# Kernel tuning notes

Hardware: AMD Instinct MI355X
Metric: run time of the kernel (lower is better)

The kernel has to match this reference:

```python
import jax, jax.numpy as jnp
import numpy as np

H, W = 512, 512          # resized_image_size
HEAT_R = 40              # heatmap_radius
OFF_R = 40               # offsetmap_radius
N_PTS = 19               # num landmarks (channels // 3)
B = 4


def _general_maps():
    # heatmap: binary disk of radius HEAT_R centered at (H, W) on a (2H, 2W) grid
    yg = jnp.arange(2 * H)[:, None]
    xg = jnp.arange(2 * W)[None, :]
    dist2 = ((yg - H) ** 2 + (xg - W) ** 2).astype(jnp.float32)
    heat = (jnp.sqrt(dist2) <= HEAT_R).astype(jnp.float32)
    # offsetmap_x: (H - row_index) / OFF_R, broadcast along columns
    off_x = jnp.broadcast_to(
        (H - jnp.arange(2 * H, dtype=jnp.float32))[:, None] / OFF_R, (2 * H, 2 * W))
    # offsetmap_y: (W - col_index) / OFF_R, broadcast along rows
    off_y = jnp.broadcast_to(
        (W - jnp.arange(2 * W, dtype=jnp.float32))[None, :] / OFF_R, (2 * H, 2 * W))
    return heat, off_x, off_y


def _crop(source, x, y):
    # rect[b, n, i, j] = source[H - y[b,n] + i, W - x[b,n] + j]
    row = (H - y)[:, :, :] if False else (H - y)[:, :, None] + jnp.arange(H)  # [B, N, H]
    col = (W - x)[:, :, None] + jnp.arange(W)                                # [B, N, W]
    return source[row[:, :, :, None], col[:, :, None, :]]                    # [B, N, H, W]


def setup_inputs() -> dict:
    key = jax.random.key(0)
    k1, k2 = jax.random.split(key)
    feature_maps = jax.random.normal(k1, (B, 3 * N_PTS, H, W), dtype=jnp.float32)
    landmarks = jax.random.randint(k2, (B, N_PTS, 2), 0, 512, dtype=jnp.int32)
    return {"feature_maps": feature_maps, "landmarks": landmarks}


def reference(feature_maps, landmarks):
    heat_map, off_x_map, off_y_map = _general_maps()
    lm = landmarks.astype(jnp.int32)
    x = jnp.clip(lm[..., 0], 1, W - 1)   # clamp_landmarks
    y = jnp.clip(lm[..., 1], 1, H - 1)

    heatmaps = _crop(heat_map, x, y)     # [B, N, H, W]
    offmap_x = _crop(off_x_map, x, y)
    offmap_y = _crop(off_y_map, x, y)

    # mask = (clamped landmarks > 0).prod(-1); always 1 after clamp but kept faithful
    mask = ((x > 0) & (y > 0)).astype(jnp.float32)[:, :, None, None]

    n = N_PTS
    ph, th = feature_maps[:, :n] * mask, heatmaps * mask
    px, tx = feature_maps[:, n:2 * n] * mask, offmap_x * mask
    py, ty = feature_maps[:, 2 * n:] * mask, offmap_y * mask

    # BCE with logits, mean reduction (numerically stable form)
    bce = jnp.mean(jnp.maximum(ph, 0.0) - ph * th + jnp.log1p(jnp.exp(-jnp.abs(ph))))

    # L1 over elements where target heatmap > 0 (masked-mean form, jit-safe)
    ind = (th > 0).astype(jnp.float32)
    cnt = jnp.sum(ind)
    lx = jnp.sum(jnp.abs(px - tx) * ind) / cnt
    ly = jnp.sum(jnp.abs(py - ty) * ind) / cnt

    return 2.0 * bce + lx + ly
```

## Files before the change

kernel.cpp:

```cpp
#include <hip/hip_runtime.h>
#include <math.h>

static constexpr int H = 512, W = 512, NPTS = 19, BATCH = 4;
static constexpr int HW = H * W;
static constexpr int NPLANES = BATCH * NPTS;
static constexpr long long TOTAL = (long long)NPLANES * HW;
static constexpr float INV_OFF = 1.0f / 40.0f;

static constexpr int BX_BULK = 16;
static constexpr int BX_DISK = 8;
static constexpr int BX      = BX_BULK + BX_DISK;
static constexpr int SITER   = (HW / 4) / (BX_BULK * 256);
static constexpr int NBULK   = BX_BULK * NPLANES;
static constexpr int NDISK   = BX_DISK * NPLANES;

__global__ __launch_bounds__(256) void homl_main(
    const float* __restrict__ fm, const int* __restrict__ lm,
    double* __restrict__ ws_)
{
    const int bn = blockIdx.y;
    const int b  = bn / NPTS;
    const int n  = bn % NPTS;

    int x = lm[bn * 2 + 0];
    int y = lm[bn * 2 + 1];
    x = min(max(x, 1), W - 1);
    y = min(max(y, 1), H - 1);

    __shared__ float redf[4][4];
    const int wave = threadIdx.x >> 6;
    const int lane = threadIdx.x & 63;

    if (blockIdx.x < BX_BULK) {
        const float* ph_base = fm + ((size_t)b * 3 * NPTS + n) * HW;
        const int v0 = blockIdx.x * (SITER * 256) + threadIdx.x;

        float bce = 0.0f;
        float4 buf[4];
        #pragma unroll
        for (int s0 = 0; s0 < 3; ++s0)
            buf[s0] = *reinterpret_cast<const float4*>(ph_base + (v0 + s0 * 256) * 4);

        #pragma unroll
        for (int s = 0; s < SITER; ++s) {
            if (s + 3 < SITER)
                buf[(s + 3) & 3] = *reinterpret_cast<const float4*>(
                    ph_base + (v0 + (s + 3) * 256) * 4);

            const int p   = (v0 + s * 256) * 4;
            const int i   = p >> 9;
            const int j   = p & (W - 1);
            const int dy  = i - y;
            const int dy2 = dy * dy;

            const float pha[4] = {buf[s & 3].x, buf[s & 3].y, buf[s & 3].z, buf[s & 3].w};
            #pragma unroll
            for (int k = 0; k < 4; ++k) {
                const int dx = j + k - x;
                const int d2 = dy2 + dx * dx;
                const float ph = pha[k];
                const float a  = fabsf(ph);
                const float sp = 0.69314718056f *
                                 log2f(1.0f + exp2f(-1.44269504089f * a));
                bce += fmaxf(ph, 0.0f) + sp;
                bce -= (d2 <= 1600) ? ph : 0.0f;
            }
        }

        #pragma unroll
        for (int off = 32; off > 0; off >>= 1) bce += __shfl_down(bce, off);
        if (lane == 0) redf[0][wave] = bce;
        __syncthreads();
        if (threadIdx.x == 0) {
            double db = 0.0;
            #pragma unroll
            for (int wv = 0; wv < 4; ++wv) db += (double)redf[0][wv];
            ws_[bn * BX_BULK + blockIdx.x] = db;
        }
    } else {
        const int dblk = blockIdx.x - BX_BULK;
        const float* px_base = fm + ((size_t)b * 3 * NPTS + NPTS + n) * HW;
        const float* py_base = fm + ((size_t)b * 3 * NPTS + 2 * NPTS + n) * HW;

        const int rbeg = dblk * 11;
        const int rcnt = min(11, 81 - rbeg);

        float lxs = 0.0f, lys = 0.0f, cntf = 0.0f;
        for (int idx = threadIdx.x; idx < rcnt * 81; idx += 256) {
            const int rr = idx / 81;
            const int cc = idx - rr * 81;
            const int dy = rbeg + rr - 40;
            const int dx = cc - 40;
            const int r  = y + dy;
            const int c  = x + dx;
            if (r >= 0 && r < H && c >= 0 && c < W && dy * dy + dx * dx <= 1600) {
                const float tx = (float)(-dy) * INV_OFF;
                const float ty = (float)(-dx) * INV_OFF;
                const size_t off = (size_t)r * W + c;
                lxs  += fabsf(px_base[off] - tx);
                lys  += fabsf(py_base[off] - ty);
                cntf += 1.0f;
            }
        }

        #pragma unroll
        for (int off = 32; off > 0; off >>= 1) {
            lxs  += __shfl_down(lxs, off);
            lys  += __shfl_down(lys, off);
            cntf += __shfl_down(cntf, off);
        }
        if (lane == 0) { redf[1][wave] = lxs; redf[2][wave] = lys; redf[3][wave] = cntf; }
        __syncthreads();
        if (threadIdx.x == 0) {
            double dxs = 0.0, dys = 0.0, dc = 0.0;
            #pragma unroll
            for (int wv = 0; wv < 4; ++wv) {
                dxs += (double)redf[1][wv];
                dys += (double)redf[2][wv];
                dc  += (double)redf[3][wv];
            }
            double4 o; o.x = dxs; o.y = dys; o.z = dc; o.w = 0.0;
            *reinterpret_cast<double4*>(ws_ + NBULK + (size_t)(bn * BX_DISK + dblk) * 4) = o;
        }
    }
}

__global__ __launch_bounds__(256) void homl_final(
    const double* __restrict__ ws_, float* __restrict__ out)
{
    double bs = 0.0, xs = 0.0, ys = 0.0, c = 0.0;
    for (int i = threadIdx.x; i < NBULK; i += 256) bs += ws_[i];
    const double* dp = ws_ + NBULK;
    for (int i = threadIdx.x; i < NDISK; i += 256) {
        xs += dp[(size_t)i * 4 + 0];
        ys += dp[(size_t)i * 4 + 1];
        c  += dp[(size_t)i * 4 + 2];
    }
    #pragma unroll
    for (int off = 32; off > 0; off >>= 1) {
        bs += __shfl_down(bs, off);
        xs += __shfl_down(xs, off);
        ys += __shfl_down(ys, off);
        c  += __shfl_down(c, off);
    }
    __shared__ double sd[4][4];
    const int wave = threadIdx.x >> 6;
    const int lane = threadIdx.x & 63;
    if (lane == 0) { sd[0][wave] = bs; sd[1][wave] = xs; sd[2][wave] = ys; sd[3][wave] = c; }
    __syncthreads();
    if (threadIdx.x == 0) {
        double tb = 0.0, txs = 0.0, tys = 0.0, tc = 0.0;
        #pragma unroll
        for (int wv = 0; wv < 4; ++wv) {
            tb += sd[0][wv]; txs += sd[1][wv]; tys += sd[2][wv]; tc += sd[3][wv];
        }
        const double bce_mean = tb / (double)TOTAL;
        out[0] = (float)(2.0 * bce_mean + txs / tc + tys / tc);
    }
}

extern "C" void kernel_launch(void* const* d_in, const int* in_sizes, int n_in,
                              void* d_out, int out_size, void* d_ws, size_t ws_size,
                              hipStream_t stream) {
    const float* fm  = (const float*)d_in[0];
    const int*   lm  = (const int*)d_in[1];
    float*       out = (float*)d_out;
    double*      ws  = (double*)d_ws;

    dim3 grid(BX, NPLANES);
    homl_main<<<grid, 256, 0, stream>>>(fm, lm, ws);
    homl_final<<<1, 256, 0, stream>>>(ws, out);
}
```

Before: 27.18 us.

## Fold disk L1 work into bulk BCE blocks and drop separate disk blocks

Removes the dedicated disk blocks and gives each of the 16 bulk blocks per plane an interleaved subset of the 81 disk rows (rows bx+16*rr). Each thread issues its two gathered px/py loads before the BCE streaming loop so their latency overlaps the bulk work, and the L1 terms are added after the loop. The per-block partials are packed into one double4 slot, which the final kernel reads with vector loads. This shrinks the grid and evens out per-block work, at the cost of extra registers and a few scattered loads in every block.

```diff
diff --git a/kernel.cpp b/kernel.cpp
--- a/kernel.cpp
+++ b/kernel.cpp
@@ -7,18 +7,16 @@
 static constexpr long long TOTAL = (long long)NPLANES * HW;
 static constexpr float INV_OFF = 1.0f / 40.0f;
 
-static constexpr int BX_BULK = 16;
-static constexpr int BX_DISK = 8;
-static constexpr int BX      = BX_BULK + BX_DISK;
-static constexpr int SITER   = (HW / 4) / (BX_BULK * 256);
-static constexpr int NBULK   = BX_BULK * NPLANES;
-static constexpr int NDISK   = BX_DISK * NPLANES;
+static constexpr int BLOCKSX = 16;
+static constexpr int SITER   = (HW / 4) / (BLOCKSX * 256);
+static constexpr int NSLOTS  = BLOCKSX * NPLANES;
 
 __global__ __launch_bounds__(256) void homl_main(
     const float* __restrict__ fm, const int* __restrict__ lm,
     double* __restrict__ ws_)
 {
     const int bn = blockIdx.y;
+    const int bx = blockIdx.x;
     const int b  = bn / NPTS;
     const int n  = bn % NPTS;
 
@@ -27,101 +25,104 @@
     x = min(max(x, 1), W - 1);
     y = min(max(y, 1), H - 1);
 
+    const float* ph_base = fm + ((size_t)b * 3 * NPTS + n) * HW;
+    const float* px_base = ph_base + (size_t)NPTS * HW;
+    const float* py_base = px_base + (size_t)NPTS * HW;
+
+    const int nrows = (bx == 0) ? 6 : 5;
+    float pxv[2], pyv[2], txv[2], tyv[2];
+    bool  val[2];
+    #pragma unroll
+    for (int t = 0; t < 2; ++t) {
+        const int idx = threadIdx.x + t * 256;
+        const int rr  = idx / 81;
+        const int cc  = idx - rr * 81;
+        const int brow = bx + 16 * rr;
+        const int dy  = brow - 40;
+        const int dx  = cc - 40;
+        const int r   = y + dy;
+        const int c   = x + dx;
+        const bool v  = (rr < nrows) && (r >= 0) && (r < H) &&
+                        (c >= 0) && (c < W) && (dy * dy + dx * dx <= 1600);
+        const size_t off = v ? ((size_t)r * W + c) : 0;
+        pxv[t] = px_base[off];
+        pyv[t] = py_base[off];
+        txv[t] = (float)(-dy) * INV_OFF;
+        tyv[t] = (float)(-dx) * INV_OFF;
+        val[t] = v;
+    }
+
+    const int v0 = bx * (SITER * 256) + threadIdx.x;
+
+    float bce = 0.0f;
+    float4 buf[4];
+    #pragma unroll
+    for (int s0 = 0; s0 < 3; ++s0)
+        buf[s0] = *reinterpret_cast<const float4*>(ph_base + (v0 + s0 * 256) * 4);
+
+    #pragma unroll
+    for (int s = 0; s < SITER; ++s) {
+        if (s + 3 < SITER)
+            buf[(s + 3) & 3] = *reinterpret_cast<const float4*>(
+                ph_base + (v0 + (s + 3) * 256) * 4);
+
+        const int p   = (v0 + s * 256) * 4;
+        const int i   = p >> 9;
+        const int j   = p & (W - 1);
+        const int dyb = i - y;
+        const int dy2 = dyb * dyb;
+
+        const float pha[4] = {buf[s & 3].x, buf[s & 3].y, buf[s & 3].z, buf[s & 3].w};
+        #pragma unroll
+        for (int k = 0; k < 4; ++k) {
+            const int dx = j + k - x;
+            const int d2 = dy2 + dx * dx;
+            const float ph = pha[k];
+            const float a  = fabsf(ph);
+            const float sp = 0.69314718056f *
+                             log2f(1.0f + exp2f(-1.44269504089f * a));
+            bce += fmaxf(ph, 0.0f) + sp;
+            bce -= (d2 <= 1600) ? ph : 0.0f;
+        }
+    }
+
+    float lxs = 0.0f, lys = 0.0f, cntf = 0.0f;
+    #pragma unroll
+    for (int t = 0; t < 2; ++t) {
+        if (val[t]) {
+            lxs  += fabsf(pxv[t] - txv[t]);
+            lys  += fabsf(pyv[t] - tyv[t]);
+            cntf += 1.0f;
+        }
+    }
+
+    #pragma unroll
+    for (int off = 32; off > 0; off >>= 1) {
+        bce  += __shfl_down(bce, off);
+        lxs  += __shfl_down(lxs, off);
+        lys  += __shfl_down(lys, off);
+        cntf += __shfl_down(cntf, off);
+    }
+
     __shared__ float redf[4][4];
     const int wave = threadIdx.x >> 6;
     const int lane = threadIdx.x & 63;
-
-    if (blockIdx.x < BX_BULK) {
-        const float* ph_base = fm + ((size_t)b * 3 * NPTS + n) * HW;
-        const int v0 = blockIdx.x * (SITER * 256) + threadIdx.x;
-
-        float bce = 0.0f;
-        float4 buf[4];
+    if (lane == 0) {
+        redf[0][wave] = bce; redf[1][wave] = lxs;
+        redf[2][wave] = lys; redf[3][wave] = cntf;
+    }
+    __syncthreads();
+    if (threadIdx.x == 0) {
+        double db = 0.0, dxs = 0.0, dys = 0.0, dc = 0.0;
         #pragma unroll
-        for (int s0 = 0; s0 < 3; ++s0)
-            buf[s0] = *reinterpret_cast<const float4*>(ph_base + (v0 + s0 * 256) * 4);
-
-        #pragma unroll
-        for (int s = 0; s < SITER; ++s) {
-            if (s + 3 < SITER)
-                buf[(s + 3) & 3] = *reinterpret_cast<const float4*>(
-                    ph_base + (v0 + (s + 3) * 256) * 4);
-
-            const int p   = (v0 + s * 256) * 4;
-            const int i   = p >> 9;
-            const int j   = p & (W - 1);
-            const int dy  = i - y;
-            const int dy2 = dy * dy;
-
-            const float pha[4] = {buf[s & 3].x, buf[s & 3].y, buf[s & 3].z, buf[s & 3].w};
-            #pragma unroll
-            for (int k = 0; k < 4; ++k) {
-                const int dx = j + k - x;
-                const int d2 = dy2 + dx * dx;
-                const float ph = pha[k];
-                const float a  = fabsf(ph);
-                const float sp = 0.69314718056f *
-                                 log2f(1.0f + exp2f(-1.44269504089f * a));
-                bce += fmaxf(ph, 0.0f) + sp;
-                bce -= (d2 <= 1600) ? ph : 0.0f;
-            }
+        for (int wv = 0; wv < 4; ++wv) {
+            db  += (double)redf[0][wv];
+            dxs += (double)redf[1][wv];
+            dys += (double)redf[2][wv];
+            dc  += (double)redf[3][wv];
         }
-
-        #pragma unroll
-        for (int off = 32; off > 0; off >>= 1) bce += __shfl_down(bce, off);
-        if (lane == 0) redf[0][wave] = bce;
-        __syncthreads();
-        if (threadIdx.x == 0) {
-            double db = 0.0;
-            #pragma unroll
-            for (int wv = 0; wv < 4; ++wv) db += (double)redf[0][wv];
-            ws_[bn * BX_BULK + blockIdx.x] = db;
-        }
-    } else {
-        const int dblk = blockIdx.x - BX_BULK;
-        const float* px_base = fm + ((size_t)b * 3 * NPTS + NPTS + n) * HW;
-        const float* py_base = fm + ((size_t)b * 3 * NPTS + 2 * NPTS + n) * HW;
-
-        const int rbeg = dblk * 11;
-        const int rcnt = min(11, 81 - rbeg);
-
-        float lxs = 0.0f, lys = 0.0f, cntf = 0.0f;
-        for (int idx = threadIdx.x; idx < rcnt * 81; idx += 256) {
-            const int rr = idx / 81;
-            const int cc = idx - rr * 81;
-            const int dy = rbeg + rr - 40;
-            const int dx = cc - 40;
-            const int r  = y + dy;
-            const int c  = x + dx;
-            if (r >= 0 && r < H && c >= 0 && c < W && dy * dy + dx * dx <= 1600) {
-                const float tx = (float)(-dy) * INV_OFF;
-                const float ty = (float)(-dx) * INV_OFF;
-                const size_t off = (size_t)r * W + c;
-                lxs  += fabsf(px_base[off] - tx);
-                lys  += fabsf(py_base[off] - ty);
-                cntf += 1.0f;
-            }
-        }
-
-        #pragma unroll
-        for (int off = 32; off > 0; off >>= 1) {
-            lxs  += __shfl_down(lxs, off);
-            lys  += __shfl_down(lys, off);
-            cntf += __shfl_down(cntf, off);
-        }
-        if (lane == 0) { redf[1][wave] = lxs; redf[2][wave] = lys; redf[3][wave] = cntf; }
-        __syncthreads();
-        if (threadIdx.x == 0) {
-            double dxs = 0.0, dys = 0.0, dc = 0.0;
-            #pragma unroll
-            for (int wv = 0; wv < 4; ++wv) {
-                dxs += (double)redf[1][wv];
-                dys += (double)redf[2][wv];
-                dc  += (double)redf[3][wv];
-            }
-            double4 o; o.x = dxs; o.y = dys; o.z = dc; o.w = 0.0;
-            *reinterpret_cast<double4*>(ws_ + NBULK + (size_t)(bn * BX_DISK + dblk) * 4) = o;
-        }
+        double4 o; o.x = db; o.y = dxs; o.z = dys; o.w = dc;
+        *reinterpret_cast<double4*>(ws_ + (size_t)(bn * BLOCKSX + bx) * 4) = o;
     }
 }
 
@@ -129,12 +130,9 @@
     const double* __restrict__ ws_, float* __restrict__ out)
 {
     double bs = 0.0, xs = 0.0, ys = 0.0, c = 0.0;
-    for (int i = threadIdx.x; i < NBULK; i += 256) bs += ws_[i];
-    const double* dp = ws_ + NBULK;
-    for (int i = threadIdx.x; i < NDISK; i += 256) {
-        xs += dp[(size_t)i * 4 + 0];
-        ys += dp[(size_t)i * 4 + 1];
-        c  += dp[(size_t)i * 4 + 2];
+    for (int i = threadIdx.x; i < NSLOTS; i += 256) {
+        const double4 p = *reinterpret_cast<const double4*>(ws_ + (size_t)i * 4);
+        bs += p.x; xs += p.y; ys += p.z; c += p.w;
     }
     #pragma unroll
     for (int off = 32; off > 0; off >>= 1) {
@@ -167,7 +165,7 @@
     float*       out = (float*)d_out;
     double*      ws  = (double*)d_ws;
 
-    dim3 grid(BX, NPLANES);
+    dim3 grid(BLOCKSX, NPLANES);
     homl_main<<<grid, 256, 0, stream>>>(fm, lm, ws);
     homl_final<<<1, 256, 0, stream>>>(ws, out);
 }
```

Result: no change. 26.93 us (-0.9%).
